# Performance work log

Measured on AMD Instinct MI355X. Metric: run time of the kernel, lower is better.

## Reference

```python
import jax, jax.numpy as jnp
import numpy as np

N_NODES = 100000
IN_DIM = 64
OUT_DIM = 64
N_EDGES = 1250000


def setup_inputs() -> dict:
    key = jax.random.key(0)
    k1, k2, k3, k4 = jax.random.split(key, 4)
    x = jax.random.normal(k1, (N_NODES, IN_DIM), dtype=jnp.float32)
    edge_index = jax.random.randint(k2, (2, N_EDGES), 0, N_NODES, dtype=jnp.int32)
    # Linear weights stored as [in, out] so y = x @ W (equivalent to torch x @ W.T)
    s = 1.0 / np.sqrt(IN_DIM)
    W1 = jax.random.uniform(k3, (IN_DIM, OUT_DIM), dtype=jnp.float32, minval=-s, maxval=s)
    W2 = jax.random.uniform(k4, (IN_DIM, OUT_DIM), dtype=jnp.float32, minval=-s, maxval=s)
    return {"x": x, "edge_index": edge_index, "W1": W1, "W2": W2}


def reference(x, edge_index, W1, W2):
    # self part: [N, out]
    self_part = x @ W1
    # transform-then-gather is mathematically identical to gather-then-transform
    # (linear map commutes with row gather) and cheaper when E > N.
    msgs = (x @ W2)[edge_index[0]]            # [E, out]
    neighbor_part = jax.ops.segment_sum(msgs, edge_index[1], num_segments=x.shape[0])
    return jax.nn.relu(self_part + neighbor_part)
```

## Files before the change

### kernel.cpp

```cpp
#include <hip/hip_runtime.h>

#define N_NODES 100000
#define N_EDGES 1250000
#define DIM 64

#define B_SHIFT 7
#define BUCKET_NODES 128
#define NBUCKETS ((N_NODES + BUCKET_NODES - 1) / BUCKET_NODES)
#define CAP 2560
#define CHUNK 2048
#define NBLK_EDGE ((N_EDGES + CHUNK - 1) / CHUNK)
#define GEMM_BLOCKS 512
#define SG_THREADS 1024

typedef __attribute__((ext_vector_type(8))) short short8;
typedef __attribute__((ext_vector_type(4))) float f32x4;

static __host__ __device__ inline size_t align256(size_t x) { return (x + 255) & ~(size_t)255; }

__device__ inline float bf16_to_f32(unsigned short u) {
  return __uint_as_float(((unsigned)u) << 16);
}
__device__ inline unsigned short f32_to_bf16(float f) {
  unsigned u = __float_as_uint(f);
  u += 0x7FFFu + ((u >> 16) & 1u);
  return (unsigned short)(u >> 16);
}

__global__ __launch_bounds__(256) void fused_gemm_partition(
    const float* __restrict__ x,
    const float* __restrict__ W1,
    const float* __restrict__ W2,
    unsigned short* __restrict__ y1b,
    unsigned short* __restrict__ y2b,
    const int* __restrict__ ei,
    int* __restrict__ gcursor,
    unsigned* __restrict__ pairs,
    int nTiles) {
  __shared__ int h[NBUCKETS];
  __shared__ int gbase[NBUCKETS];

  if (blockIdx.x < NBLK_EDGE) {
    const int nE = N_EDGES;
    for (int i = threadIdx.x; i < NBUCKETS; i += 256) h[i] = 0;
    __syncthreads();
    int base = blockIdx.x * CHUNK;
    int end = min(base + CHUNK, nE);
    for (int e = base + (int)threadIdx.x; e < end; e += 256)
      atomicAdd(&h[ei[nE + e] >> B_SHIFT], 1);
    __syncthreads();
    for (int i = threadIdx.x; i < NBUCKETS; i += 256) {
      int c = h[i];
      gbase[i] = c ? atomicAdd(&gcursor[i], c) : 0;
      h[i] = 0;
    }
    __syncthreads();
    for (int e = base + (int)threadIdx.x; e < end; e += 256) {
      int dst = ei[nE + e];
      int src = ei[e];
      int b = dst >> B_SHIFT;
      int pos = gbase[b] + atomicAdd(&h[b], 1);
      if (pos < CAP)
        pairs[b * CAP + pos] = (unsigned)src | ((unsigned)(dst & (BUCKET_NODES - 1)) << 17);
    }
  } else {
    int lane = threadIdx.x & 63;
    int wave = ((blockIdx.x - NBLK_EDGE) * 256 + (int)threadIdx.x) >> 6;
    int nWaves = GEMM_BLOCKS * 4;
    int m = lane & 15;
    int q = lane >> 4;

    short8 wf[2][2][4];
#pragma unroll
    for (int w = 0; w < 2; ++w) {
      const float* W = w ? W2 : W1;
#pragma unroll
      for (int kh = 0; kh < 2; ++kh)
#pragma unroll
        for (int nt = 0; nt < 4; ++nt) {
          short8 f;
#pragma unroll
          for (int j = 0; j < 8; ++j) {
            int k = kh * 32 + q * 8 + j;
            f[j] = (short)f32_to_bf16(W[k * DIM + nt * 16 + m]);
          }
          wf[w][kh][nt] = f;
        }
    }

    for (int t = wave; t < nTiles; t += nWaves) {
      int rowBase = t * 16;
      const float* xr = x + (size_t)(rowBase + m) * DIM + q * 8;

      short8 af[2];
#pragma unroll
      for (int kh = 0; kh < 2; ++kh) {
        float4 u0 = *(const float4*)(xr + kh * 32);
        float4 u1 = *(const float4*)(xr + kh * 32 + 4);
        short8 f;
        f[0] = (short)f32_to_bf16(u0.x);
        f[1] = (short)f32_to_bf16(u0.y);
        f[2] = (short)f32_to_bf16(u0.z);
        f[3] = (short)f32_to_bf16(u0.w);
        f[4] = (short)f32_to_bf16(u1.x);
        f[5] = (short)f32_to_bf16(u1.y);
        f[6] = (short)f32_to_bf16(u1.z);
        f[7] = (short)f32_to_bf16(u1.w);
        af[kh] = f;
      }

#pragma unroll
      for (int w = 0; w < 2; ++w) {
        unsigned short* Y = w ? y2b : y1b;
        f32x4 acc[4];
#pragma unroll
        for (int nt = 0; nt < 4; ++nt) {
          acc[nt] = (f32x4){0.f, 0.f, 0.f, 0.f};
          acc[nt] = __builtin_amdgcn_mfma_f32_16x16x32_bf16(af[0], wf[w][0][nt], acc[nt], 0, 0, 0);
          acc[nt] = __builtin_amdgcn_mfma_f32_16x16x32_bf16(af[1], wf[w][1][nt], acc[nt], 0, 0, 0);
        }
#pragma unroll
        for (int nt = 0; nt < 4; ++nt)
#pragma unroll
          for (int r = 0; r < 4; ++r)
            Y[(size_t)(rowBase + q * 4 + r) * DIM + nt * 16 + m] = f32_to_bf16(acc[nt][r]);
      }
    }
  }
}

__global__ __launch_bounds__(SG_THREADS) void sort_gather(
    const unsigned* __restrict__ pairs,
    const int* __restrict__ gcursor,
    const unsigned short* __restrict__ y1b,
    const unsigned short* __restrict__ y2b,
    float* __restrict__ out,
    int nNodesTotal) {
  __shared__ unsigned buf[CAP];
  __shared__ unsigned sorted[CAP];
  __shared__ int cnt[BUCKET_NODES];
  __shared__ int scn[BUCKET_NODES];
  __shared__ int cur[BUCKET_NODES];

  int b = blockIdx.x;
  int n = min(gcursor[b], CAP);
  int tid = threadIdx.x;
  const unsigned* pb = pairs + (size_t)b * CAP;

  if (tid < BUCKET_NODES) cnt[tid] = 0;
  __syncthreads();
  for (int i = tid; i < n; i += SG_THREADS) {
    unsigned w = pb[i];
    buf[i] = w;
    atomicAdd(&cnt[(w >> 17) & 127], 1);
  }
  __syncthreads();

  int v = 0;
  if (tid < BUCKET_NODES) { v = cnt[tid]; scn[tid] = v; }
  __syncthreads();
#pragma unroll
  for (int off = 1; off < BUCKET_NODES; off <<= 1) {
    int t = 0;
    if (tid < BUCKET_NODES && tid >= off) t = scn[tid - off];
    __syncthreads();
    if (tid < BUCKET_NODES) scn[tid] += t;
    __syncthreads();
  }
  if (tid < BUCKET_NODES) cur[tid] = scn[tid] - v;
  __syncthreads();

  for (int i = tid; i < n; i += SG_THREADS) {
    unsigned w = buf[i];
    int l = (int)((w >> 17) & 127);
    int p = atomicAdd(&cur[l], 1);
    sorted[p] = w & 0x1FFFFu;
  }
  __syncthreads();

  int lane = tid & 63;
  int wv = tid >> 6;
  int g = lane >> 4;
  int c16 = lane & 15;
  const ushort4* y2q = (const ushort4*)y2b;
  const ushort4* y1q = (const ushort4*)y1b;
  int nodeBase = b << B_SHIFT;
  int numNodes = min(BUCKET_NODES, nNodesTotal - nodeBase);

  for (int ln = wv; ln < numNodes; ln += (SG_THREADS / 64)) {
    int deg = cnt[ln];
    int begin = scn[ln] - deg;
    int end = begin + deg;

    float ax = 0.f, ay = 0.f, az = 0.f, aw = 0.f;
    float bx = 0.f, by = 0.f, bz = 0.f, bw = 0.f;
    int e = begin;
    for (; e + 7 < end; e += 8) {
      int s0 = (int)sorted[e + g];
      int s1 = (int)sorted[e + 4 + g];
      ushort4 u0 = y2q[(size_t)s0 * 16 + c16];
      ushort4 u1 = y2q[(size_t)s1 * 16 + c16];
      ax += bf16_to_f32(u0.x); ay += bf16_to_f32(u0.y);
      az += bf16_to_f32(u0.z); aw += bf16_to_f32(u0.w);
      bx += bf16_to_f32(u1.x); by += bf16_to_f32(u1.y);
      bz += bf16_to_f32(u1.z); bw += bf16_to_f32(u1.w);
    }
    for (; e + 3 < end; e += 4) {
      int s = (int)sorted[e + g];
      ushort4 u = y2q[(size_t)s * 16 + c16];
      ax += bf16_to_f32(u.x); ay += bf16_to_f32(u.y);
      az += bf16_to_f32(u.z); aw += bf16_to_f32(u.w);
    }
    if (e + g < end) {
      int s = (int)sorted[e + g];
      ushort4 u = y2q[(size_t)s * 16 + c16];
      ax += bf16_to_f32(u.x); ay += bf16_to_f32(u.y);
      az += bf16_to_f32(u.z); aw += bf16_to_f32(u.w);
    }

    float sx = ax + bx, sy = ay + by, sz = az + bz, sw = aw + bw;
    sx += __shfl_xor(sx, 16, 64);
    sy += __shfl_xor(sy, 16, 64);
    sz += __shfl_xor(sz, 16, 64);
    sw += __shfl_xor(sw, 16, 64);
    sx += __shfl_xor(sx, 32, 64);
    sy += __shfl_xor(sy, 32, 64);
    sz += __shfl_xor(sz, 32, 64);
    sw += __shfl_xor(sw, 32, 64);

    if (lane < 16) {
      int node = nodeBase + ln;
      ushort4 s1v = y1q[(size_t)node * 16 + lane];
      float4 o;
      o.x = fmaxf(bf16_to_f32(s1v.x) + sx, 0.0f);
      o.y = fmaxf(bf16_to_f32(s1v.y) + sy, 0.0f);
      o.z = fmaxf(bf16_to_f32(s1v.z) + sz, 0.0f);
      o.w = fmaxf(bf16_to_f32(s1v.w) + sw, 0.0f);
      ((float4*)out)[(size_t)node * 16 + lane] = o;
    }
  }
}

__global__ __launch_bounds__(256) void gemm_simple(
    const float* __restrict__ x, const float* __restrict__ W1, const float* __restrict__ W2,
    float* __restrict__ y1, unsigned short* __restrict__ y2b, int n) {
  int row = blockIdx.x * blockDim.x + threadIdx.x;
  if (row >= n) return;
  float xv[DIM];
  const float4* xr = (const float4*)(x + (size_t)row * DIM);
#pragma unroll
  for (int i = 0; i < DIM / 4; ++i) {
    float4 t = xr[i];
    xv[4 * i] = t.x; xv[4 * i + 1] = t.y; xv[4 * i + 2] = t.z; xv[4 * i + 3] = t.w;
  }
#pragma unroll
  for (int m = 0; m < 2; ++m) {
    const float* W = (m == 0) ? W1 : W2;
#pragma unroll
    for (int cc = 0; cc < DIM; cc += 16) {
      float acc[16];
#pragma unroll
      for (int c2 = 0; c2 < 16; ++c2) acc[c2] = 0.0f;
      for (int k = 0; k < DIM; ++k) {
        float xk = xv[k];
        const float* wr = W + k * DIM + cc;
#pragma unroll
        for (int c2 = 0; c2 < 16; ++c2) acc[c2] = fmaf(xk, wr[c2], acc[c2]);
      }
      if (m == 0) {
        for (int c2 = 0; c2 < 16; ++c2) y1[(size_t)row * DIM + cc + c2] = acc[c2];
      } else {
        for (int c2 = 0; c2 < 16; ++c2) y2b[(size_t)row * DIM + cc + c2] = f32_to_bf16(acc[c2]);
      }
    }
  }
}

__global__ __launch_bounds__(256) void scatter_add(const int* __restrict__ ei,
                                                   const unsigned short* __restrict__ y2b,
                                                   float* __restrict__ out, int nE) {
  int gid = blockIdx.x * blockDim.x + threadIdx.x;
  int edge = gid >> 6;
  int lane = threadIdx.x & 63;
  if (edge >= nE) return;
  int src = __builtin_amdgcn_readfirstlane(ei[edge]);
  int dst = __builtin_amdgcn_readfirstlane(ei[nE + edge]);
  atomicAdd(&out[(size_t)dst * DIM + lane], bf16_to_f32(y2b[(size_t)src * DIM + lane]));
}

__global__ __launch_bounds__(256) void relu_inplace(float* __restrict__ out, int n4) {
  int i = blockIdx.x * blockDim.x + threadIdx.x;
  if (i >= n4) return;
  float4* p = (float4*)out;
  float4 v = p[i];
  v.x = fmaxf(v.x, 0.0f);
  v.y = fmaxf(v.y, 0.0f);
  v.z = fmaxf(v.z, 0.0f);
  v.w = fmaxf(v.w, 0.0f);
  p[i] = v;
}

extern "C" void kernel_launch(void* const* d_in, const int* in_sizes, int n_in,
                              void* d_out, int out_size, void* d_ws, size_t ws_size,
                              hipStream_t stream) {
  const float* x  = (const float*)d_in[0];
  const int*   ei = (const int*)d_in[1];
  const float* W1 = (const float*)d_in[2];
  const float* W2 = (const float*)d_in[3];
  float* out = (float*)d_out;

  char* ws = (char*)d_ws;
  size_t off = 0;
  unsigned short* y2b = (unsigned short*)(ws + off); off += align256((size_t)N_NODES * DIM * sizeof(unsigned short));
  unsigned short* y1b = (unsigned short*)(ws + off); off += align256((size_t)N_NODES * DIM * sizeof(unsigned short));
  int* gcursor = (int*)(ws + off);                   off += align256((size_t)NBUCKETS * sizeof(int));
  unsigned* pairs = (unsigned*)(ws + off);           off += align256((size_t)NBUCKETS * CAP * sizeof(unsigned));
  size_t required = off;

  if (ws_size >= required) {
    hipMemsetAsync(gcursor, 0, (size_t)NBUCKETS * sizeof(int), stream);
    fused_gemm_partition<<<NBLK_EDGE + GEMM_BLOCKS, 256, 0, stream>>>(
        x, W1, W2, y1b, y2b, ei, gcursor, pairs, N_NODES / 16);
    sort_gather<<<NBUCKETS, SG_THREADS, 0, stream>>>(pairs, gcursor, y1b, y2b, out, N_NODES);
  } else {
    {
      int blocks = (N_NODES + 255) / 256;
      gemm_simple<<<blocks, 256, 0, stream>>>(x, W1, W2, out, y2b, N_NODES);
    }
    {
      long long threads = (long long)N_EDGES * 64;
      int blocks = (int)((threads + 255) / 256);
      scatter_add<<<blocks, 256, 0, stream>>>(ei, y2b, out, N_EDGES);
    }
    {
      int n4 = N_NODES * DIM / 4;
      int blocks = (n4 + 255) / 256;
      relu_inplace<<<blocks, 256, 0, stream>>>(out, n4);
    }
  }
}
```

Before: 157.8 us.

## Split fused kernel and locally sort edges by bucket before scattering

Splits the fused GEMM/partition kernel into two separate launches. The partition kernel now counts each chunk's edges per bucket, prefix-scans the counts, stages the edges in shared memory in bucket order, and writes them out in that order. Consecutive threads then write to contiguous runs of the global pairs array instead of scattered addresses, which should coalesce the writes. In exchange it adds shared-memory scan barriers, uses more LDS per block, and loses the overlap between the GEMM and partition work that the fused kernel had.

```diff
diff --git a/kernel.cpp b/kernel.cpp
--- a/kernel.cpp
+++ b/kernel.cpp
@@ -8,8 +8,9 @@
 #define BUCKET_NODES 128
 #define NBUCKETS ((N_NODES + BUCKET_NODES - 1) / BUCKET_NODES)
 #define CAP 2560
-#define CHUNK 2048
-#define NBLK_EDGE ((N_EDGES + CHUNK - 1) / CHUNK)
+#define P_CHUNK 4096
+#define P_THREADS 512
+#define NBLK_P ((N_EDGES + P_CHUNK - 1) / P_CHUNK)
 #define GEMM_BLOCKS 512
 #define SG_THREADS 1024
 
@@ -27,104 +28,141 @@
   return (unsigned short)(u >> 16);
 }
 
-__global__ __launch_bounds__(256) void fused_gemm_partition(
+__global__ __launch_bounds__(P_THREADS) void partition_sorted(
+    const int* __restrict__ ei,
+    int* __restrict__ gcursor,
+    unsigned* __restrict__ pairs) {
+  __shared__ int h[NBUCKETS];
+  __shared__ int scn[NBUCKETS];
+  __shared__ int cur[NBUCKETS];
+  __shared__ int gbase[NBUCKETS];
+  __shared__ int tsum[P_THREADS];
+  __shared__ unsigned sval[P_CHUNK];
+  __shared__ int saddr[P_CHUNK];
+
+  const int nE = N_EDGES;
+  int tid = threadIdx.x;
+  int base = blockIdx.x * P_CHUNK;
+  int end = min(base + P_CHUNK, nE);
+  int cntE = end - base;
+
+  for (int i = tid; i < NBUCKETS; i += P_THREADS) h[i] = 0;
+  __syncthreads();
+  for (int e = base + tid; e < end; e += P_THREADS)
+    atomicAdd(&h[ei[nE + e] >> B_SHIFT], 1);
+  __syncthreads();
+
+  {
+    int b0 = tid * 2;
+    int l0 = 0, l1 = 0, s = 0;
+    if (b0 < NBUCKETS)     { l0 = s; s += h[b0]; }
+    if (b0 + 1 < NBUCKETS) { l1 = s; s += h[b0 + 1]; }
+    tsum[tid] = s;
+    __syncthreads();
+    for (int off = 1; off < P_THREADS; off <<= 1) {
+      int t = (tid >= off) ? tsum[tid - off] : 0;
+      __syncthreads();
+      tsum[tid] += t;
+      __syncthreads();
+    }
+    int p = tsum[tid] - s;
+    if (b0 < NBUCKETS)     scn[b0] = p + l0;
+    if (b0 + 1 < NBUCKETS) scn[b0 + 1] = p + l1;
+  }
+  __syncthreads();
+
+  for (int i = tid; i < NBUCKETS; i += P_THREADS) {
+    int c = h[i];
+    gbase[i] = c ? atomicAdd(&gcursor[i], c) : 0;
+    cur[i] = scn[i];
+  }
+  __syncthreads();
+
+  for (int e = base + tid; e < end; e += P_THREADS) {
+    int dst = ei[nE + e];
+    int src = ei[e];
+    int b = dst >> B_SHIFT;
+    int lp = atomicAdd(&cur[b], 1);
+    int inb = lp - scn[b];
+    int gpos = gbase[b] + inb;
+    sval[lp] = (unsigned)src | ((unsigned)(dst & (BUCKET_NODES - 1)) << 17);
+    saddr[lp] = (gpos < CAP) ? (b * CAP + gpos) : -1;
+  }
+  __syncthreads();
+
+  for (int j = tid; j < cntE; j += P_THREADS) {
+    int a = saddr[j];
+    if (a >= 0) pairs[a] = sval[j];
+  }
+}
+
+__global__ __launch_bounds__(256) void gemm_mfma(
     const float* __restrict__ x,
     const float* __restrict__ W1,
     const float* __restrict__ W2,
     unsigned short* __restrict__ y1b,
     unsigned short* __restrict__ y2b,
-    const int* __restrict__ ei,
-    int* __restrict__ gcursor,
-    unsigned* __restrict__ pairs,
     int nTiles) {
-  __shared__ int h[NBUCKETS];
-  __shared__ int gbase[NBUCKETS];
-
-  if (blockIdx.x < NBLK_EDGE) {
-    const int nE = N_EDGES;
-    for (int i = threadIdx.x; i < NBUCKETS; i += 256) h[i] = 0;
-    __syncthreads();
-    int base = blockIdx.x * CHUNK;
-    int end = min(base + CHUNK, nE);
-    for (int e = base + (int)threadIdx.x; e < end; e += 256)
-      atomicAdd(&h[ei[nE + e] >> B_SHIFT], 1);
-    __syncthreads();
-    for (int i = threadIdx.x; i < NBUCKETS; i += 256) {
-      int c = h[i];
-      gbase[i] = c ? atomicAdd(&gcursor[i], c) : 0;
-      h[i] = 0;
-    }
-    __syncthreads();
-    for (int e = base + (int)threadIdx.x; e < end; e += 256) {
-      int dst = ei[nE + e];
-      int src = ei[e];
-      int b = dst >> B_SHIFT;
-      int pos = gbase[b] + atomicAdd(&h[b], 1);
-      if (pos < CAP)
-        pairs[b * CAP + pos] = (unsigned)src | ((unsigned)(dst & (BUCKET_NODES - 1)) << 17);
-    }
-  } else {
-    int lane = threadIdx.x & 63;
-    int wave = ((blockIdx.x - NBLK_EDGE) * 256 + (int)threadIdx.x) >> 6;
-    int nWaves = GEMM_BLOCKS * 4;
-    int m = lane & 15;
-    int q = lane >> 4;
-
-    short8 wf[2][2][4];
+  int lane = threadIdx.x & 63;
+  int wave = (blockIdx.x * 256 + (int)threadIdx.x) >> 6;
+  int nWaves = GEMM_BLOCKS * 4;
+  int m = lane & 15;
+  int q = lane >> 4;
+
+  short8 wf[2][2][4];
+#pragma unroll
+  for (int w = 0; w < 2; ++w) {
+    const float* W = w ? W2 : W1;
+#pragma unroll
+    for (int kh = 0; kh < 2; ++kh)
+#pragma unroll
+      for (int nt = 0; nt < 4; ++nt) {
+        short8 f;
+#pragma unroll
+        for (int j = 0; j < 8; ++j) {
+          int k = kh * 32 + q * 8 + j;
+          f[j] = (short)f32_to_bf16(W[k * DIM + nt * 16 + m]);
+        }
+        wf[w][kh][nt] = f;
+      }
+  }
+
+  for (int t = wave; t < nTiles; t += nWaves) {
+    int rowBase = t * 16;
+    const float* xr = x + (size_t)(rowBase + m) * DIM + q * 8;
+
+    short8 af[2];
+#pragma unroll
+    for (int kh = 0; kh < 2; ++kh) {
+      float4 u0 = *(const float4*)(xr + kh * 32);
+      float4 u1 = *(const float4*)(xr + kh * 32 + 4);
+      short8 f;
+      f[0] = (short)f32_to_bf16(u0.x);
+      f[1] = (short)f32_to_bf16(u0.y);
+      f[2] = (short)f32_to_bf16(u0.z);
+      f[3] = (short)f32_to_bf16(u0.w);
+      f[4] = (short)f32_to_bf16(u1.x);
+      f[5] = (short)f32_to_bf16(u1.y);
+      f[6] = (short)f32_to_bf16(u1.z);
+      f[7] = (short)f32_to_bf16(u1.w);
+      af[kh] = f;
+    }
+
 #pragma unroll
     for (int w = 0; w < 2; ++w) {
-      const float* W = w ? W2 : W1;
-#pragma unroll
-      for (int kh = 0; kh < 2; ++kh)
-#pragma unroll
-        for (int nt = 0; nt < 4; ++nt) {
-          short8 f;
-#pragma unroll
-          for (int j = 0; j < 8; ++j) {
-            int k = kh * 32 + q * 8 + j;
-            f[j] = (short)f32_to_bf16(W[k * DIM + nt * 16 + m]);
-          }
-          wf[w][kh][nt] = f;
-        }
-    }
-
-    for (int t = wave; t < nTiles; t += nWaves) {
-      int rowBase = t * 16;
-      const float* xr = x + (size_t)(rowBase + m) * DIM + q * 8;
-
-      short8 af[2];
-#pragma unroll
-      for (int kh = 0; kh < 2; ++kh) {
-        float4 u0 = *(const float4*)(xr + kh * 32);
-        float4 u1 = *(const float4*)(xr + kh * 32 + 4);
-        short8 f;
-        f[0] = (short)f32_to_bf16(u0.x);
-        f[1] = (short)f32_to_bf16(u0.y);
-        f[2] = (short)f32_to_bf16(u0.z);
-        f[3] = (short)f32_to_bf16(u0.w);
-        f[4] = (short)f32_to_bf16(u1.x);
-        f[5] = (short)f32_to_bf16(u1.y);
-        f[6] = (short)f32_to_bf16(u1.z);
-        f[7] = (short)f32_to_bf16(u1.w);
-        af[kh] = f;
+      unsigned short* Y = w ? y2b : y1b;
+      f32x4 acc[4];
+#pragma unroll
+      for (int nt = 0; nt < 4; ++nt) {
+        acc[nt] = (f32x4){0.f, 0.f, 0.f, 0.f};
+        acc[nt] = __builtin_amdgcn_mfma_f32_16x16x32_bf16(af[0], wf[w][0][nt], acc[nt], 0, 0, 0);
+        acc[nt] = __builtin_amdgcn_mfma_f32_16x16x32_bf16(af[1], wf[w][1][nt], acc[nt], 0, 0, 0);
       }
-
-#pragma unroll
-      for (int w = 0; w < 2; ++w) {
-        unsigned short* Y = w ? y2b : y1b;
-        f32x4 acc[4];
-#pragma unroll
-        for (int nt = 0; nt < 4; ++nt) {
-          acc[nt] = (f32x4){0.f, 0.f, 0.f, 0.f};
-          acc[nt] = __builtin_amdgcn_mfma_f32_16x16x32_bf16(af[0], wf[w][0][nt], acc[nt], 0, 0, 0);
-          acc[nt] = __builtin_amdgcn_mfma_f32_16x16x32_bf16(af[1], wf[w][1][nt], acc[nt], 0, 0, 0);
-        }
-#pragma unroll
-        for (int nt = 0; nt < 4; ++nt)
-#pragma unroll
-          for (int r = 0; r < 4; ++r)
-            Y[(size_t)(rowBase + q * 4 + r) * DIM + nt * 16 + m] = f32_to_bf16(acc[nt][r]);
-      }
+#pragma unroll
+      for (int nt = 0; nt < 4; ++nt)
+#pragma unroll
+        for (int r = 0; r < 4; ++r)
+          Y[(size_t)(rowBase + q * 4 + r) * DIM + nt * 16 + m] = f32_to_bf16(acc[nt][r]);
     }
   }
 }
@@ -319,8 +357,8 @@
 
   if (ws_size >= required) {
     hipMemsetAsync(gcursor, 0, (size_t)NBUCKETS * sizeof(int), stream);
-    fused_gemm_partition<<<NBLK_EDGE + GEMM_BLOCKS, 256, 0, stream>>>(
-        x, W1, W2, y1b, y2b, ei, gcursor, pairs, N_NODES / 16);
+    partition_sorted<<<NBLK_P, P_THREADS, 0, stream>>>(ei, gcursor, pairs);
+    gemm_mfma<<<GEMM_BLOCKS, 256, 0, stream>>>(x, W1, W2, y1b, y2b, N_NODES / 16);
     sort_gather<<<NBUCKETS, SG_THREADS, 0, stream>>>(pairs, gcursor, y1b, y2b, out, N_NODES);
   } else {
     {
```

Result: faster. 148.7 us (-5.8%).
